# Kernel tuning notes

Hardware: AMD Instinct MI355X
Metric: run time of the kernel (lower is better)

Reference implementation:

```python
import jax, jax.numpy as jnp
import numpy as np

B, N, H, C = 8, 128, 768, 5


def setup_inputs() -> dict:
    key = jax.random.key(0)
    k0, k1, k2, k3 = jax.random.split(key, 4)
    h = jax.random.normal(k0, (B, N, H), dtype=jnp.float32)
    # torch nn.Linear(4H, H): out = x @ W.T + b; we store Wcat = W.T with shape [4H, H]
    Wcat = jax.random.normal(k1, (4 * H, H), dtype=jnp.float32) * 0.02
    bW = jnp.zeros((H,), dtype=jnp.float32)
    h_hat = jax.random.normal(k2, (H,), dtype=jnp.float32)
    Wout = jax.random.normal(k3, (H, C), dtype=jnp.float32) * 0.02
    bout = jnp.zeros((C,), dtype=jnp.float32)
    return {"h": h, "Wcat": Wcat, "bW": bW, "h_hat": h_hat, "Wout": Wout, "bout": bout}


def reference(h, Wcat, bW, h_hat, Wout, bout):
    n = h.shape[1]
    W1, W2, W3, W4 = jnp.split(Wcat, 4, axis=0)  # each [H, H]
    # span order matches the torch double loop: i in range(N), j in range(i, N)
    ii, jj = jnp.triu_indices(n)  # P = n(n+1)/2
    # cat([hi,hj,hi-hj,hi*hj]) @ Wcat == hi@(W1+W3) + hj@(W2-W3) + (hi*hj)@W4
    A = jnp.einsum('bnh,hk->bnk', h, W1 + W3)   # [B, N, H]
    Bm = jnp.einsum('bnh,hk->bnk', h, W2 - W3)  # [B, N, H]
    prod = h[:, ii, :] * h[:, jj, :]            # [B, P, H]
    spans = jnp.tanh(A[:, ii, :] + Bm[:, jj, :]
                     + jnp.einsum('bph,hk->bpk', prod, W4) + bW)  # [B, P, H]
    # InterpretationLayer: attention pooling over spans
    alpha = jax.nn.softmax(jnp.einsum('bph,h->bp', spans, h_hat), axis=1)
    h_tilde = jnp.einsum('bp,bph->bh', alpha, spans)  # [B, H]
    logits = h_tilde @ Wout + bout                    # [B, C]
    return jax.nn.log_softmax(logits, axis=1)
```

## Files before the change

kernel.cpp:

```cpp
#include <hip/hip_runtime.h>
#include <hip/hip_bf16.h>


#define B_ 8
#define N_ 128
#define H_ 768
#define C_ 5
#define P_ 8256
#define TP 64
#define NBLK 129

typedef short bf16x8 __attribute__((ext_vector_type(8)));
typedef float f32x4 __attribute__((ext_vector_type(4)));

__device__ __forceinline__ float bf2f(unsigned short u){
  union { unsigned u; float f; } v; v.u = ((unsigned)u) << 16; return v.f;
}
__device__ __forceinline__ unsigned short f2bf(float f){
  union { float f; unsigned u; } v; v.f = f;
  unsigned r = v.u + 0x7FFFu + ((v.u >> 16) & 1u);
  return (unsigned short)(r >> 16);
}
__device__ __forceinline__ float tanh_fast(float x){
  float e = __expf(2.f * x);
  return 1.f - 2.f / (e + 1.f);
}
__device__ __forceinline__ int lds_off(int row, int k){
  return row * (H_ * 2) + ((k * 2) ^ ((row & 7) << 4));
}


#define PH_BLKS 3072
#define PW_BLKS 288
#define PR_BLKS 33

__global__ void prep(const float* __restrict__ h, const float* __restrict__ Wcat,
                     unsigned short* __restrict__ hb,
                     unsigned short* __restrict__ Wsum,
                     unsigned short* __restrict__ Wdif,
                     unsigned short* __restrict__ W4s,
                     int* __restrict__ ii, int* __restrict__ jj){
  const int bid = blockIdx.x;
  if (bid < PH_BLKS){
    int idx = bid * 256 + threadIdx.x;
    hb[idx] = f2bf(h[idx]);
  } else if (bid < PH_BLKS + PW_BLKS){
    int idx = (bid - PH_BLKS) * 256 + threadIdx.x;
    int o = idx / H_, col = idx % H_;
    bf16x8 vs, vd, v4;
    #pragma unroll
    for (int e = 0; e < 8; e++){
      int hrow = o * 8 + e;
      float w1 = Wcat[hrow * H_ + col];
      float w2 = Wcat[(H_ + hrow) * H_ + col];
      float w3 = Wcat[(2 * H_ + hrow) * H_ + col];
      float w4 = Wcat[(3 * H_ + hrow) * H_ + col];
      vs[e] = (short)f2bf(w1 + w3);
      vd[e] = (short)f2bf(w2 - w3);
      v4[e] = (short)f2bf(w4);
    }
    int pbase = (o * H_ + col) * 8;
    *(bf16x8*)(Wsum + pbase) = vs;
    *(bf16x8*)(Wdif + pbase) = vd;
    *(bf16x8*)(W4s + pbase)  = v4;
  } else {
    int p = (bid - PH_BLKS - PW_BLKS) * 256 + threadIdx.x;
    if (p < P_){
      int i = 0, off = 0;
      while (off + (N_ - i) <= p){ off += (N_ - i); i++; }
      ii[p] = i; jj[p] = i + (p - off);
    }
  }
}


__global__ __launch_bounds__(512, 4) void coef_gemm(
    const unsigned short* __restrict__ hb,
    const unsigned short* __restrict__ Wsum,
    const unsigned short* __restrict__ Wdif,
    const float* __restrict__ bW,
    float* __restrict__ Acoef, float* __restrict__ Bcoef){
  const int sel = blockIdx.y;
  const unsigned short* Wp = sel ? Wdif : Wsum;
  float* out = sel ? Bcoef : Acoef;
  const int growb = blockIdx.x * 16;

  __shared__ char As[16 * H_ * 2];

  const int tid = threadIdx.x;
  {
    int r = tid >> 5;
    int c = tid & 31;
    const unsigned short* src = hb + (growb + r) * H_;
    #pragma unroll
    for (int kk = 0; kk < 3; kk++){
      int k = kk * 256 + c * 8;
      bf16x8 v = *(const bf16x8*)(src + k);
      *(bf16x8*)(As + lds_off(r, k)) = v;
    }
  }
  __syncthreads();

  const int lane = tid & 63;
  const int wn = tid >> 6;
  const int hi = lane >> 4;
  const int l15 = lane & 15;
  const int colbase = wn * 96 + l15;

  f32x4 acc[6] = {};

  const bf16x8* wp = (const bf16x8*)Wp + hi * H_ + colbase;
  bf16x8 bc0 = wp[0], bc1 = wp[16], bc2 = wp[32], bc3 = wp[48], bc4 = wp[64], bc5 = wp[80];
  wp += 4 * H_;
  for (int step = 0; step < 24; ++step){
    bf16x8 bn0 = wp[0], bn1 = wp[16], bn2 = wp[32], bn3 = wp[48], bn4 = wp[64], bn5 = wp[80];
    wp += 4 * H_;
    bf16x8 a = *(const bf16x8*)(As + lds_off(l15, step * 32 + hi * 8));
    acc[0] = __builtin_amdgcn_mfma_f32_16x16x32_bf16(a, bc0, acc[0], 0, 0, 0);
    acc[1] = __builtin_amdgcn_mfma_f32_16x16x32_bf16(a, bc1, acc[1], 0, 0, 0);
    acc[2] = __builtin_amdgcn_mfma_f32_16x16x32_bf16(a, bc2, acc[2], 0, 0, 0);
    acc[3] = __builtin_amdgcn_mfma_f32_16x16x32_bf16(a, bc3, acc[3], 0, 0, 0);
    acc[4] = __builtin_amdgcn_mfma_f32_16x16x32_bf16(a, bc4, acc[4], 0, 0, 0);
    acc[5] = __builtin_amdgcn_mfma_f32_16x16x32_bf16(a, bc5, acc[5], 0, 0, 0);
    bc0 = bn0; bc1 = bn1; bc2 = bn2; bc3 = bn3; bc4 = bn4; bc5 = bn5;
  }

  #pragma unroll
  for (int ni = 0; ni < 6; ni++){
    int col = colbase + ni * 16;
    float bw = (sel == 0) ? bW[col] : 0.f;
    #pragma unroll
    for (int r = 0; r < 4; r++){
      int grow = growb + hi * 4 + r;
      out[grow * H_ + col] = acc[ni][r] + bw;
    }
  }
}


__global__ __launch_bounds__(1024)
__attribute__((amdgpu_waves_per_eu(4, 4)))
void spans_fused(
    const unsigned short* __restrict__ hb,
    const float* __restrict__ Acoef,
    const float* __restrict__ Bcoef,
    const unsigned short* __restrict__ W4s,
    const float* __restrict__ hhat,
    const int* __restrict__ ii,
    const int* __restrict__ jj,
    float* __restrict__ pm, float* __restrict__ pl, float* __restrict__ pacc){
  __shared__ char As[TP * H_ * 2];
  __shared__ int iis[TP], jjs[TP];
  __shared__ float sbuf[16][TP];
  __shared__ float wbuf[TP];

  const int bid = blockIdx.x;
  const int b = bid / NBLK;
  const int p0 = (bid % NBLK) * TP;
  const int tid = threadIdx.x;

  if (tid < TP){ iis[tid] = ii[p0 + tid]; jjs[tid] = jj[p0 + tid]; }
  __syncthreads();

  {
    int r = tid >> 4;
    int c = tid & 15;
    const unsigned short* hp = hb + (b * N_ + iis[r]) * H_;
    const unsigned short* hq = hb + (b * N_ + jjs[r]) * H_;
    #pragma unroll
    for (int kk = 0; kk < 6; kk++){
      int k = kk * 128 + c * 8;
      bf16x8 va = *(const bf16x8*)(hp + k);
      bf16x8 vb = *(const bf16x8*)(hq + k);
      bf16x8 vp;
      #pragma unroll
      for (int e = 0; e < 8; e++)
        vp[e] = (short)f2bf(bf2f((unsigned short)va[e]) * bf2f((unsigned short)vb[e]));
      *(bf16x8*)(As + lds_off(r, k)) = vp;
    }
  }

  const int lane = tid & 63;
  const int wave = tid >> 6;
  const int hi = lane >> 4;
  const int l15 = lane & 15;
  const int colbase = wave * 48 + l15;

  f32x4 acc[4][3];
  #pragma unroll
  for (int mi = 0; mi < 4; mi++){
    #pragma unroll
    for (int r = 0; r < 4; r++){
      int rowl = mi * 16 + hi * 4 + r;
      const float* ap = Acoef + (b * N_ + iis[rowl]) * H_ + colbase;
      const float* bp = Bcoef + (b * N_ + jjs[rowl]) * H_ + colbase;
      #pragma unroll
      for (int ni = 0; ni < 3; ni++)
        acc[mi][ni][r] = ap[ni * 16] + bp[ni * 16];
    }
  }
  __syncthreads();

  const bf16x8* wp = (const bf16x8*)W4s + hi * H_ + colbase;
  bf16x8 bc0 = wp[0], bc1 = wp[16], bc2 = wp[32];
  wp += 4 * H_;
  for (int step = 0; step < 24; ++step){
    bf16x8 bn0 = wp[0], bn1 = wp[16], bn2 = wp[32];
    wp += 4 * H_;
    const int kb = step * 32 + hi * 8;
    bf16x8 a0 = *(const bf16x8*)(As + lds_off(     l15, kb));
    bf16x8 a1 = *(const bf16x8*)(As + lds_off(16 + l15, kb));
    bf16x8 a2 = *(const bf16x8*)(As + lds_off(32 + l15, kb));
    bf16x8 a3 = *(const bf16x8*)(As + lds_off(48 + l15, kb));
    acc[0][0] = __builtin_amdgcn_mfma_f32_16x16x32_bf16(a0, bc0, acc[0][0], 0, 0, 0);
    acc[1][0] = __builtin_amdgcn_mfma_f32_16x16x32_bf16(a1, bc0, acc[1][0], 0, 0, 0);
    acc[2][0] = __builtin_amdgcn_mfma_f32_16x16x32_bf16(a2, bc0, acc[2][0], 0, 0, 0);
    acc[3][0] = __builtin_amdgcn_mfma_f32_16x16x32_bf16(a3, bc0, acc[3][0], 0, 0, 0);
    acc[0][1] = __builtin_amdgcn_mfma_f32_16x16x32_bf16(a0, bc1, acc[0][1], 0, 0, 0);
    acc[1][1] = __builtin_amdgcn_mfma_f32_16x16x32_bf16(a1, bc1, acc[1][1], 0, 0, 0);
    acc[2][1] = __builtin_amdgcn_mfma_f32_16x16x32_bf16(a2, bc1, acc[2][1], 0, 0, 0);
    acc[3][1] = __builtin_amdgcn_mfma_f32_16x16x32_bf16(a3, bc1, acc[3][1], 0, 0, 0);
    acc[0][2] = __builtin_amdgcn_mfma_f32_16x16x32_bf16(a0, bc2, acc[0][2], 0, 0, 0);
    acc[1][2] = __builtin_amdgcn_mfma_f32_16x16x32_bf16(a1, bc2, acc[1][2], 0, 0, 0);
    acc[2][2] = __builtin_amdgcn_mfma_f32_16x16x32_bf16(a2, bc2, acc[2][2], 0, 0, 0);
    acc[3][2] = __builtin_amdgcn_mfma_f32_16x16x32_bf16(a3, bc2, acc[3][2], 0, 0, 0);
    bc0 = bn0; bc1 = bn1; bc2 = bn2;
  }

  float sc[4][4];
  #pragma unroll
  for (int mi = 0; mi < 4; mi++)
    #pragma unroll
    for (int r = 0; r < 4; r++) sc[mi][r] = 0.f;

  #pragma unroll
  for (int ni = 0; ni < 3; ni++){
    float hh = hhat[colbase + ni * 16];
    #pragma unroll
    for (int mi = 0; mi < 4; mi++){
      #pragma unroll
      for (int r = 0; r < 4; r++){
        float s = tanh_fast(acc[mi][ni][r]);
        acc[mi][ni][r] = s;
        sc[mi][r] += s * hh;
      }
    }
  }
  #pragma unroll
  for (int mi = 0; mi < 4; mi++)
    #pragma unroll
    for (int r = 0; r < 4; r++){
      float v = sc[mi][r];
      v += __shfl_xor(v, 1); v += __shfl_xor(v, 2);
      v += __shfl_xor(v, 4); v += __shfl_xor(v, 8);
      sc[mi][r] = v;
    }
  if (l15 == 0){
    #pragma unroll
    for (int mi = 0; mi < 4; mi++)
      #pragma unroll
      for (int r = 0; r < 4; r++)
        sbuf[wave][mi * 16 + hi * 4 + r] = sc[mi][r];
  }
  __syncthreads();

  if (tid < TP){
    float s = 0.f;
    #pragma unroll
    for (int w = 0; w < 16; w++) s += sbuf[w][tid];
    float m = s;
    #pragma unroll
    for (int off = 1; off < 64; off <<= 1) m = fmaxf(m, __shfl_xor(m, off));
    float w = __expf(s - m);
    float l = w;
    #pragma unroll
    for (int off = 1; off < 64; off <<= 1) l += __shfl_xor(l, off);
    wbuf[tid] = w;
    if (tid == 0){ pm[bid] = m; pl[bid] = l; }
  }
  __syncthreads();

  #pragma unroll
  for (int ni = 0; ni < 3; ni++){
    float wa = 0.f;
    #pragma unroll
    for (int mi = 0; mi < 4; mi++)
      #pragma unroll
      for (int r = 0; r < 4; r++){
        int rowl = mi * 16 + hi * 4 + r;
        wa += wbuf[rowl] * acc[mi][ni][r];
      }
    wa += __shfl_xor(wa, 16);
    wa += __shfl_xor(wa, 32);
    if (lane < 16) pacc[bid * H_ + colbase + ni * 16] = wa;
  }
}


__global__ void merge1(
    const float* __restrict__ pm, const float* __restrict__ pl,
    const float* __restrict__ pacc, float* __restrict__ htg){
  __shared__ float ebuf[NBLK];
  __shared__ float Msh, invLsh;
  __shared__ float part[128];
  const int b = blockIdx.x;
  const int ch = blockIdx.y;
  const int tid = threadIdx.x;

  if (tid < 64){
    float m = -3.4e38f;
    for (int t = tid; t < NBLK; t += 64) m = fmaxf(m, pm[b * NBLK + t]);
    #pragma unroll
    for (int off = 1; off < 64; off <<= 1) m = fmaxf(m, __shfl_xor(m, off));
    float l = 0.f;
    for (int t = tid; t < NBLK; t += 64) l += pl[b * NBLK + t] * __expf(pm[b * NBLK + t] - m);
    #pragma unroll
    for (int off = 1; off < 64; off <<= 1) l += __shfl_xor(l, off);
    if (tid == 0){ Msh = m; invLsh = 1.f / l; }
  }
  __syncthreads();
  if (tid < NBLK) ebuf[tid] = __expf(pm[b * NBLK + tid] - Msh);
  __syncthreads();
  const int col = ch * 128 + (tid & 127);
  const int half = tid >> 7;
  float a = 0.f;
  for (int t = half; t < NBLK; t += 2) a += pacc[(b * NBLK + t) * H_ + col] * ebuf[t];
  if (half) part[tid & 127] = a;
  __syncthreads();
  if (!half) htg[b * H_ + col] = (a + part[tid]) * invLsh;
}


__global__ void merge2(
    const float* __restrict__ htg,
    const float* __restrict__ Wout, const float* __restrict__ bout,
    float* __restrict__ outp){
  const int b = blockIdx.x;
  const int lane = threadIdx.x;
  float a[C_] = {};
  for (int k = lane; k < H_; k += 64){
    float hv = htg[b * H_ + k];
    #pragma unroll
    for (int c = 0; c < C_; c++) a[c] += hv * Wout[k * C_ + c];
  }
  #pragma unroll
  for (int c = 0; c < C_; c++){
    #pragma unroll
    for (int off = 1; off < 64; off <<= 1) a[c] += __shfl_xor(a[c], off);
  }
  if (lane == 0){
    float lg[C_];
    #pragma unroll
    for (int c = 0; c < C_; c++) lg[c] = a[c] + bout[c];
    float mx = lg[0];
    #pragma unroll
    for (int c = 1; c < C_; c++) mx = fmaxf(mx, lg[c]);
    float s = 0.f;
    #pragma unroll
    for (int c = 0; c < C_; c++) s += __expf(lg[c] - mx);
    float ls = __logf(s) + mx;
    #pragma unroll
    for (int c = 0; c < C_; c++) outp[b * C_ + c] = lg[c] - ls;
  }
}


extern "C" void kernel_launch(void* const* d_in, const int* in_sizes, int n_in,
                              void* d_out, int out_size, void* d_ws, size_t ws_size,
                              hipStream_t stream){
  const float* h    = (const float*)d_in[0];
  const float* Wcat = (const float*)d_in[1];
  const float* bW   = (const float*)d_in[2];
  const float* hhat = (const float*)d_in[3];
  const float* Wout = (const float*)d_in[4];
  const float* bout = (const float*)d_in[5];
  float* outp = (float*)d_out;

  unsigned short* hb   = (unsigned short*)d_ws;
  unsigned short* Wsum = hb + 786432;
  unsigned short* Wdif = Wsum + 589824;
  unsigned short* W4s  = Wdif + 589824;
  float* Acoef = (float*)(W4s + 589824);
  float* Bcoef = Acoef + 786432;
  int* iiA = (int*)(Bcoef + 786432);
  int* jjA = iiA + P_;
  float* pm = (float*)(jjA + P_);
  float* pl = pm + (B_ * NBLK);
  float* pacc = pl + (B_ * NBLK);
  float* htg  = pacc + (B_ * NBLK * H_);

  prep<<<PH_BLKS + PW_BLKS + PR_BLKS, 256, 0, stream>>>(h, Wcat, hb, Wsum, Wdif, W4s, iiA, jjA);
  coef_gemm<<<dim3(64, 2), 512, 0, stream>>>(hb, Wsum, Wdif, bW, Acoef, Bcoef);
  spans_fused<<<B_ * NBLK, 1024, 0, stream>>>(hb, Acoef, Bcoef, W4s, hhat, iiA, jjA, pm, pl, pacc);
  merge1<<<dim3(B_, 6), 256, 0, stream>>>(pm, pl, pacc, htg);
  merge2<<<B_, 64, 0, stream>>>(htg, Wout, bout, outp);
}
```

Baseline: 183.6 us.

## Deepen W4 prefetch, use packed bf16 convert, widen LDS swizzle in spans kernel

The spans kernel's K loop is fully unrolled with a three-slot register ring for W4 fragments, prefetching two steps ahead instead of one. The first two W4 loads are issued before the barrier so they overlap LDS fill. The elementwise product now packs pairs into bf16 with v_cvt_pk_bf16_f32 instead of software rounding. The LDS XOR swizzle widens from 8 to 16 rows, and the launch bounds attribute changes form. Extra prefetch registers could raise register pressure at the fixed occupancy target.

Result: faster. 174.8 us (-4.8%).

```diff
diff --git a/kernel.cpp b/kernel.cpp
--- a/kernel.cpp
+++ b/kernel.cpp
@@ -9,6 +9,7 @@
 #define P_ 8256
 #define TP 64
 #define NBLK 129
+#define NSTEP 24
 
 typedef short bf16x8 __attribute__((ext_vector_type(8)));
 typedef float f32x4 __attribute__((ext_vector_type(4)));
@@ -25,8 +26,20 @@
   float e = __expf(2.f * x);
   return 1.f - 2.f / (e + 1.f);
 }
+__device__ __forceinline__ bf16x8 prodpack(bf16x8 x, bf16x8 y){
+  union { bf16x8 v; unsigned u[4]; } o;
+  #pragma unroll
+  for (int e2 = 0; e2 < 4; e2++){
+    float p0 = bf2f((unsigned short)x[e2*2])   * bf2f((unsigned short)y[e2*2]);
+    float p1 = bf2f((unsigned short)x[e2*2+1]) * bf2f((unsigned short)y[e2*2+1]);
+    unsigned pk;
+    asm volatile("v_cvt_pk_bf16_f32 %0, %1, %2" : "=v"(pk) : "v"(p0), "v"(p1));
+    o.u[e2] = pk;
+  }
+  return o.v;
+}
 __device__ __forceinline__ int lds_off(int row, int k){
-  return row * (H_ * 2) + ((k * 2) ^ ((row & 7) << 4));
+  return row * (H_ * 2) + ((k * 2) ^ ((row & 15) << 4));
 }
 
 
@@ -138,8 +151,7 @@
 }
 
 
-__global__ __launch_bounds__(1024)
-__attribute__((amdgpu_waves_per_eu(4, 4)))
+__global__ __launch_bounds__(1024, 4)
 void spans_fused(
     const unsigned short* __restrict__ hb,
     const float* __restrict__ Acoef,
@@ -172,11 +184,7 @@
       int k = kk * 128 + c * 8;
       bf16x8 va = *(const bf16x8*)(hp + k);
       bf16x8 vb = *(const bf16x8*)(hq + k);
-      bf16x8 vp;
-      #pragma unroll
-      for (int e = 0; e < 8; e++)
-        vp[e] = (short)f2bf(bf2f((unsigned short)va[e]) * bf2f((unsigned short)vb[e]));
-      *(bf16x8*)(As + lds_off(r, k)) = vp;
+      *(bf16x8*)(As + lds_off(r, k)) = prodpack(va, vb);
     }
   }
 
@@ -199,32 +207,37 @@
         acc[mi][ni][r] = ap[ni * 16] + bp[ni * 16];
     }
   }
-  __syncthreads();
 
   const bf16x8* wp = (const bf16x8*)W4s + hi * H_ + colbase;
-  bf16x8 bc0 = wp[0], bc1 = wp[16], bc2 = wp[32];
-  wp += 4 * H_;
-  for (int step = 0; step < 24; ++step){
-    bf16x8 bn0 = wp[0], bn1 = wp[16], bn2 = wp[32];
-    wp += 4 * H_;
-    const int kb = step * 32 + hi * 8;
+  bf16x8 bs[3][3];
+  #pragma unroll
+  for (int s = 0; s < 2; s++)
+    #pragma unroll
+    for (int ni = 0; ni < 3; ni++)
+      bs[s][ni] = wp[s * 4 * H_ + ni * 16];
+
+  __syncthreads();
+
+  #pragma unroll
+  for (int t = 0; t < NSTEP; ++t){
+    if (t + 2 < NSTEP){
+      #pragma unroll
+      for (int ni = 0; ni < 3; ni++)
+        bs[(t + 2) % 3][ni] = wp[(t + 2) * 4 * H_ + ni * 16];
+    }
+    const int kb = t * 32 + hi * 8;
     bf16x8 a0 = *(const bf16x8*)(As + lds_off(     l15, kb));
     bf16x8 a1 = *(const bf16x8*)(As + lds_off(16 + l15, kb));
     bf16x8 a2 = *(const bf16x8*)(As + lds_off(32 + l15, kb));
     bf16x8 a3 = *(const bf16x8*)(As + lds_off(48 + l15, kb));
-    acc[0][0] = __builtin_amdgcn_mfma_f32_16x16x32_bf16(a0, bc0, acc[0][0], 0, 0, 0);
-    acc[1][0] = __builtin_amdgcn_mfma_f32_16x16x32_bf16(a1, bc0, acc[1][0], 0, 0, 0);
-    acc[2][0] = __builtin_amdgcn_mfma_f32_16x16x32_bf16(a2, bc0, acc[2][0], 0, 0, 0);
-    acc[3][0] = __builtin_amdgcn_mfma_f32_16x16x32_bf16(a3, bc0, acc[3][0], 0, 0, 0);
-    acc[0][1] = __builtin_amdgcn_mfma_f32_16x16x32_bf16(a0, bc1, acc[0][1], 0, 0, 0);
-    acc[1][1] = __builtin_amdgcn_mfma_f32_16x16x32_bf16(a1, bc1, acc[1][1], 0, 0, 0);
-    acc[2][1] = __builtin_amdgcn_mfma_f32_16x16x32_bf16(a2, bc1, acc[2][1], 0, 0, 0);
-    acc[3][1] = __builtin_amdgcn_mfma_f32_16x16x32_bf16(a3, bc1, acc[3][1], 0, 0, 0);
-    acc[0][2] = __builtin_amdgcn_mfma_f32_16x16x32_bf16(a0, bc2, acc[0][2], 0, 0, 0);
-    acc[1][2] = __builtin_amdgcn_mfma_f32_16x16x32_bf16(a1, bc2, acc[1][2], 0, 0, 0);
-    acc[2][2] = __builtin_amdgcn_mfma_f32_16x16x32_bf16(a2, bc2, acc[2][2], 0, 0, 0);
-    acc[3][2] = __builtin_amdgcn_mfma_f32_16x16x32_bf16(a3, bc2, acc[3][2], 0, 0, 0);
-    bc0 = bn0; bc1 = bn1; bc2 = bn2;
+    #pragma unroll
+    for (int ni = 0; ni < 3; ni++){
+      bf16x8 bfr = bs[t % 3][ni];
+      acc[0][ni] = __builtin_amdgcn_mfma_f32_16x16x32_bf16(a0, bfr, acc[0][ni], 0, 0, 0);
+      acc[1][ni] = __builtin_amdgcn_mfma_f32_16x16x32_bf16(a1, bfr, acc[1][ni], 0, 0, 0);
+      acc[2][ni] = __builtin_amdgcn_mfma_f32_16x16x32_bf16(a2, bfr, acc[2][ni], 0, 0, 0);
+      acc[3][ni] = __builtin_amdgcn_mfma_f32_16x16x32_bf16(a3, bfr, acc[3][ni], 0, 0, 0);
+    }
   }
 
   float sc[4][4];
```
